# Kernel tuning notes

Measured on AMD Instinct MI355X. Metric: run time of the kernel, lower is better.

Reference implementation:

```python
import jax, jax.numpy as jnp
import numpy as np

B, S, HID = 1, 2048, 2048
H, KVH, HD = 16, 8, 128          # query heads, kv heads, head_dim = HID//H
N_REP = H // KVH                 # GQA expansion factor
EPS = 1e-6
THETA = 1e6
SCALING = HD ** (-0.5)           # note: original DIVIDES scores by this (bug kept)


def setup_inputs() -> dict:
    key = jax.random.key(0)
    ks = jax.random.split(key, 5)
    hidden_states = jax.random.normal(ks[0], (B, S, HID), jnp.float32)
    std = 0.02
    wq = jax.random.normal(ks[1], (HID, H * HD), jnp.float32) * std
    wk = jax.random.normal(ks[2], (HID, KVH * HD), jnp.float32) * std
    wv = jax.random.normal(ks[3], (HID, KVH * HD), jnp.float32) * std
    wo = jax.random.normal(ks[4], (H * HD, HID), jnp.float32) * std
    # RoPE tables as in Qwen3: inv_freq over even dims, emb = [freqs, freqs]
    pos = np.arange(S, dtype=np.float64)
    inv_freq = THETA ** (-np.arange(0, HD, 2, dtype=np.float64) / HD)
    freqs = pos[:, None] * inv_freq[None, :]            # [S, HD/2]
    emb = np.concatenate([freqs, freqs], axis=-1)       # [S, HD]
    cos = jnp.asarray(np.cos(emb)[None], jnp.float32)   # [1, S, HD]
    sin = jnp.asarray(np.sin(emb)[None], jnp.float32)
    return {"hidden_states": hidden_states, "cos": cos, "sin": sin,
            "wq": wq, "wk": wk, "wv": wv, "wo": wo}


def _rmsnorm(x):
    # weightless RMSNorm (the module's RMSNorm never applies .weight)
    return x * jax.lax.rsqrt(jnp.mean(x * x, axis=-1, keepdims=True) + EPS)


def _rotate_half(x):
    x1, x2 = jnp.split(x, 2, axis=-1)
    return jnp.concatenate([-x2, x1], axis=-1)


def reference(hidden_states, cos, sin, wq, wk, wv, wo):
    # projections + per-head QK RMSNorm, then [B,H,S,D] layout
    q = _rmsnorm((hidden_states @ wq).reshape(B, S, H, HD)).transpose(0, 2, 1, 3)
    k = _rmsnorm((hidden_states @ wk).reshape(B, S, KVH, HD)).transpose(0, 2, 1, 3)
    v = (hidden_states @ wv).reshape(B, S, KVH, HD).transpose(0, 2, 1, 3)
    # RoPE (cos/sin unsqueezed at head dim)
    c = cos[:, None, :, :]   # [B,1,S,HD]
    s = sin[:, None, :, :]
    q = q * c + _rotate_half(q) * s
    k = k * c + _rotate_half(k) * s
    # GQA repeat_kv: each kv head repeated N_REP consecutive times
    k = jnp.repeat(k, N_REP, axis=1)   # [B,H,S,HD]
    v = jnp.repeat(v, N_REP, axis=1)
    # faithful: scores DIVIDED by head_dim**-0.5 (i.e. * sqrt(HD)); no causal mask
    scores = jnp.einsum('bhqd,bhkd->bhqk', q, k) / SCALING
    probs = jax.nn.softmax(scores, axis=-1)
    attn = jnp.einsum('bhqk,bhkd->bhqd', probs, v)
    out = attn.transpose(0, 2, 1, 3).reshape(B, S, H * HD) @ wo
    return out
```

## Files before the change

kernel.cpp:

```cpp
#include <hip/hip_runtime.h>
#include <hip/hip_bf16.h>
#include <math.h>

#define S 2048
#define HID 2048
#define NH 16
#define KVH 8
#define HD 128
#define EPS 1e-6f
#define QK_SCALE 11.313708498984760390f

typedef __attribute__((ext_vector_type(8))) short s16x8;
typedef __attribute__((ext_vector_type(4))) float f32x4;

__device__ __forceinline__ unsigned short f2bf(float f) {
  __hip_bfloat16 h = __float2bfloat16(f);
  return *(unsigned short*)&h;
}
__device__ __forceinline__ float bf2f(unsigned short u) {
  unsigned int x = ((unsigned int)u) << 16;
  return __builtin_bit_cast(float, x);
}

__device__ __forceinline__ void gload16(const void* g, void* l) {
  __builtin_amdgcn_global_load_lds(
      (const __attribute__((address_space(1))) void*)g,
      (__attribute__((address_space(3))) void*)l, 16, 0, 0);
}

__global__ __launch_bounds__(256) void f32_to_bf16_split(const float* __restrict__ in,
                                                         unsigned short* __restrict__ hi,
                                                         unsigned short* __restrict__ lo,
                                                         int n4) {
  const int i = blockIdx.x * 256 + threadIdx.x;
  if (i < n4) {
    const float4 v = *(const float4*)(in + (size_t)i * 4);
    ushort4 h, l;
    h.x = f2bf(v.x); l.x = f2bf(v.x - bf2f(h.x));
    h.y = f2bf(v.y); l.y = f2bf(v.y - bf2f(h.y));
    h.z = f2bf(v.z); l.z = f2bf(v.z - bf2f(h.z));
    h.w = f2bf(v.w); l.w = f2bf(v.w - bf2f(h.w));
    *(ushort4*)(hi + (size_t)i * 4) = h;
    *(ushort4*)(lo + (size_t)i * 4) = l;
  }
}

__global__ __launch_bounds__(256) void transpose_to_bf16(const float* __restrict__ in,
                                                         unsigned short* __restrict__ out,
                                                         int K, int N) {
  __shared__ float t[64][65];
  const int n0 = blockIdx.x * 64;
  const int k0 = blockIdx.y * 64;
  const int tid = threadIdx.x;

  for (int idx = tid; idx < 64 * 16; idx += 256) {
    const int r = idx >> 4;
    const int c4 = (idx & 15) * 4;
    const float4 v = *(const float4*)(in + (size_t)(k0 + r) * N + n0 + c4);
    t[r][c4 + 0] = v.x; t[r][c4 + 1] = v.y; t[r][c4 + 2] = v.z; t[r][c4 + 3] = v.w;
  }
  __syncthreads();
  for (int idx = tid; idx < 64 * 16; idx += 256) {
    const int a = idx >> 4;
    const int b4 = (idx & 15) * 4;
    ushort4 u;
    u.x = f2bf(t[b4 + 0][a]); u.y = f2bf(t[b4 + 1][a]);
    u.z = f2bf(t[b4 + 2][a]); u.w = f2bf(t[b4 + 3][a]);
    *(ushort4*)(out + (size_t)(n0 + a) * K + k0 + b4) = u;
  }
}

__global__ __launch_bounds__(256) void transpose_to_bf16_split(const float* __restrict__ in,
                                                               unsigned short* __restrict__ ohi,
                                                               unsigned short* __restrict__ olo,
                                                               int K, int N) {
  __shared__ float t[64][65];
  const int n0 = blockIdx.x * 64;
  const int k0 = blockIdx.y * 64;
  const int tid = threadIdx.x;

  for (int idx = tid; idx < 64 * 16; idx += 256) {
    const int r = idx >> 4;
    const int c4 = (idx & 15) * 4;
    const float4 v = *(const float4*)(in + (size_t)(k0 + r) * N + n0 + c4);
    t[r][c4 + 0] = v.x; t[r][c4 + 1] = v.y; t[r][c4 + 2] = v.z; t[r][c4 + 3] = v.w;
  }
  __syncthreads();
  for (int idx = tid; idx < 64 * 16; idx += 256) {
    const int a = idx >> 4;
    const int b4 = (idx & 15) * 4;
    ushort4 h, l;
#pragma unroll
    for (int q = 0; q < 4; ++q) {
      const float v = t[b4 + q][a];
      const unsigned short hu = f2bf(v);
      const unsigned short lu = f2bf(v - bf2f(hu));
      ((unsigned short*)&h)[q] = hu;
      ((unsigned short*)&l)[q] = lu;
    }
    *(ushort4*)(ohi + (size_t)(n0 + a) * K + k0 + b4) = h;
    *(ushort4*)(olo + (size_t)(n0 + a) * K + k0 + b4) = l;
  }
}

#define BK 32

__global__ __launch_bounds__(256) void gemm_split_bt64(const unsigned short* __restrict__ Ahi,
                                                       const unsigned short* __restrict__ Alo,
                                                       const unsigned short* __restrict__ Bhi,
                                                       const unsigned short* __restrict__ Blo,
                                                       float* __restrict__ C,
                                                       int M, int N, int K, int ldc) {
  __shared__ unsigned short AsH[128 * BK];
  __shared__ unsigned short AsL[128 * BK];
  __shared__ unsigned short BsH[64 * BK];
  __shared__ unsigned short BsL[64 * BK];

  const int tid = threadIdx.x;
  const int lane = tid & 63;
  const int wave = tid >> 6;
  const int m0 = blockIdx.y * 128;
  const int n0 = blockIdx.x * 64;

  const int qm = (wave >> 1) * 64;
  const int qn = (wave & 1) * 32;
  const int l15 = lane & 15;
  const int quad = lane >> 4;

  const int st_row = lane >> 2;
  const int st_col = (lane & 3) * 8;

  f32x4 acc[4][2] = {};

  for (int k0 = 0; k0 < K; k0 += BK) {
#pragma unroll
    for (int p = 0; p < 2; ++p) {
      const int rb = p * 64 + wave * 16;
      const size_t aoff = (size_t)(m0 + rb + st_row) * K + k0 + st_col;
      gload16(Ahi + aoff, &AsH[rb * BK]);
      gload16(Alo + aoff, &AsL[rb * BK]);
    }
    {
      const int rb = wave * 16;
      const size_t boff = (size_t)(n0 + rb + st_row) * K + k0 + st_col;
      gload16(Bhi + boff, &BsH[rb * BK]);
      gload16(Blo + boff, &BsL[rb * BK]);
    }
    __syncthreads();

    s16x8 ah[4], al[4], bh[2], bl[2];
#pragma unroll
    for (int i = 0; i < 4; ++i) {
      const int ro = (qm + i * 16 + l15) * BK + quad * 8;
      ah[i] = *(const s16x8*)&AsH[ro];
      al[i] = *(const s16x8*)&AsL[ro];
    }
#pragma unroll
    for (int j = 0; j < 2; ++j) {
      const int ro = (qn + j * 16 + l15) * BK + quad * 8;
      bh[j] = *(const s16x8*)&BsH[ro];
      bl[j] = *(const s16x8*)&BsL[ro];
    }
#pragma unroll
    for (int i = 0; i < 4; ++i)
#pragma unroll
      for (int j = 0; j < 2; ++j) {
        acc[i][j] = __builtin_amdgcn_mfma_f32_16x16x32_bf16(ah[i], bh[j], acc[i][j], 0, 0, 0);
        acc[i][j] = __builtin_amdgcn_mfma_f32_16x16x32_bf16(ah[i], bl[j], acc[i][j], 0, 0, 0);
        acc[i][j] = __builtin_amdgcn_mfma_f32_16x16x32_bf16(al[i], bh[j], acc[i][j], 0, 0, 0);
      }
    __syncthreads();
  }

#pragma unroll
  for (int i = 0; i < 4; ++i) {
    const int row_base = m0 + qm + i * 16 + quad * 4;
#pragma unroll
    for (int j = 0; j < 2; ++j) {
      const int col = n0 + qn + j * 16 + l15;
#pragma unroll
      for (int r = 0; r < 4; ++r)
        C[(size_t)(row_base + r) * ldc + col] = acc[i][j][r];
    }
  }
}

template <int MODE, typename OT>
__global__ __launch_bounds__(256) void gemm_bf16_6464(const unsigned short* __restrict__ A,
                                                      const unsigned short* __restrict__ Bt,
                                                      OT* __restrict__ C,
                                                      int M, int N, int K, int ldc) {
  __shared__ unsigned short As[64 * BK];
  __shared__ unsigned short Bs[64 * BK];

  const int tid = threadIdx.x;
  const int lane = tid & 63;
  const int wave = tid >> 6;
  const int m0 = blockIdx.y * 64;
  const int n0 = blockIdx.x * 64;

  const int qm = (wave >> 1) * 32;
  const int qn = (wave & 1) * 32;
  const int l15 = lane & 15;
  const int quad = lane >> 4;

  const int st_row = lane >> 2;
  const int st_col = (lane & 3) * 8;

  f32x4 acc[2][2] = {};

  for (int k0 = 0; k0 < K; k0 += BK) {
    {
      const int rb = wave * 16;
      gload16(A + (size_t)(m0 + rb + st_row) * K + k0 + st_col, &As[rb * BK]);
      gload16(Bt + (size_t)(n0 + rb + st_row) * K + k0 + st_col, &Bs[rb * BK]);
    }
    __syncthreads();

    s16x8 a[2], b[2];
#pragma unroll
    for (int i = 0; i < 2; ++i)
      a[i] = *(const s16x8*)&As[(qm + i * 16 + l15) * BK + quad * 8];
#pragma unroll
    for (int j = 0; j < 2; ++j)
      b[j] = *(const s16x8*)&Bs[(qn + j * 16 + l15) * BK + quad * 8];
#pragma unroll
    for (int i = 0; i < 2; ++i)
#pragma unroll
      for (int j = 0; j < 2; ++j)
        acc[i][j] = __builtin_amdgcn_mfma_f32_16x16x32_bf16(a[i], b[j], acc[i][j], 0, 0, 0);
    __syncthreads();
  }

#pragma unroll
  for (int i = 0; i < 2; ++i) {
    const int row_base = m0 + qm + i * 16 + quad * 4;
#pragma unroll
    for (int j = 0; j < 2; ++j) {
      const int col = n0 + qn + j * 16 + l15;
      if constexpr (MODE == 0) {
#pragma unroll
        for (int r = 0; r < 4; ++r)
          C[(size_t)(row_base + r) * ldc + col] = acc[i][j][r];
      } else {
        ushort4 u;
        u.x = f2bf(acc[i][j][0]); u.y = f2bf(acc[i][j][1]);
        u.z = f2bf(acc[i][j][2]); u.w = f2bf(acc[i][j][3]);
        *(ushort4*)((unsigned short*)C + (size_t)col * ldc + row_base) = u;
      }
    }
  }
}

__global__ __launch_bounds__(256) void rmsnorm_rope_split(const float* __restrict__ qk,
                                                          const float* __restrict__ cosb,
                                                          const float* __restrict__ sinb,
                                                          unsigned short* __restrict__ qh,
                                                          unsigned short* __restrict__ ql,
                                                          unsigned short* __restrict__ kh,
                                                          unsigned short* __restrict__ kl) {
  const int s = blockIdx.x;
  const int wave = threadIdx.x >> 6;
  const int lane = threadIdx.x & 63;
  const int hh = blockIdx.y * 4 + wave;
  const bool is_q = (hh < 16);
  const int col = is_q ? hh * HD : 2048 + (hh - 16) * HD;

  const float* row = qk + (size_t)s * 3072 + col;
  const float x1 = row[lane];
  const float x2 = row[lane + 64];

  float ss = x1 * x1 + x2 * x2;
  ss += __shfl_xor(ss, 1);
  ss += __shfl_xor(ss, 2);
  ss += __shfl_xor(ss, 4);
  ss += __shfl_xor(ss, 8);
  ss += __shfl_xor(ss, 16);
  ss += __shfl_xor(ss, 32);
  const float r = rsqrtf(ss / 128.f + EPS);

  const float c = cosb[(size_t)s * HD + lane];
  const float sn = sinb[(size_t)s * HD + lane];
  float o1 = x1 * r * c - x2 * r * sn;
  float o2 = x2 * r * c + x1 * r * sn;
  if (is_q) { o1 *= QK_SCALE; o2 *= QK_SCALE; }

  const unsigned short h1 = f2bf(o1), l1 = f2bf(o1 - bf2f(h1));
  const unsigned short h2 = f2bf(o2), l2 = f2bf(o2 - bf2f(h2));
  if (is_q) {
    const size_t base = (size_t)s * 2048 + hh * HD + lane;
    qh[base] = h1; ql[base] = l1;
    qh[base + 64] = h2; ql[base + 64] = l2;
  } else {
    const size_t base = (size_t)s * 1024 + (hh - 16) * HD + lane;
    kh[base] = h1; kl[base] = l1;
    kh[base + 64] = h2; kl[base + 64] = l2;
  }
}

#define FA_N 64
#define FA_NT (S / FA_N)

__global__ __launch_bounds__(512, 4) void attn_flash_mfma(const unsigned short* __restrict__ qh,
                                                          const unsigned short* __restrict__ ql,
                                                          const unsigned short* __restrict__ kh,
                                                          const unsigned short* __restrict__ kl,
                                                          const unsigned short* __restrict__ vt,
                                                          unsigned short* __restrict__ out) {
  const int h = blockIdx.y;
  const int kvh = h >> 1;
  const int m0 = blockIdx.x * 64;
  const int tid = threadIdx.x;
  const int lane = tid & 63;
  const int wave = tid >> 6;
  const int rg = wave >> 1;
  const int kg = wave & 1;
  const int l15 = lane & 15;
  const int quad = lane >> 4;

  __shared__ char smem[59392];
  unsigned short* Kh = (unsigned short*)(smem);
  unsigned short* Kl = (unsigned short*)(smem + 16384);
  unsigned short* Vt = (unsigned short*)(smem + 32768);
  unsigned short* Pt = (unsigned short*)(smem + 49152) + wave * 640;

  auto STAGE = [&](int nt) {
#pragma unroll
    for (int p = 0; p < 2; ++p) {
      const int kr = wave * 8 + p * 4 + (lane >> 4);
      const size_t ksrc = (size_t)(nt + kr) * 1024 + kvh * HD + ((lane & 15) ^ (kr & 15)) * 8;
      gload16(kh + ksrc, Kh + (wave * 8 + p * 4) * 128);
      gload16(kl + ksrc, Kl + (wave * 8 + p * 4) * 128);
      const int d = wave * 16 + p * 8 + (lane >> 3);
      const size_t vsrc = (size_t)(kvh * HD + d) * 2048 + nt + ((lane & 7) ^ (d & 7)) * 8;
      gload16(vt + vsrc, Vt + (wave * 16 + p * 8) * 64);
    }
  };

  s16x8 qah[4], qal[4];
  {
    const int qrow = m0 + rg * 16 + l15;
#pragma unroll
    for (int ks = 0; ks < 4; ++ks) {
      const size_t off = (size_t)qrow * 2048 + h * HD + ks * 32 + quad * 8;
      qah[ks] = *(const s16x8*)(qh + off);
      qal[ks] = *(const s16x8*)(ql + off);
    }
  }

  f32x4 O[8] = {};
  float m_i[4], l_i[4];
#pragma unroll
  for (int r = 0; r < 4; ++r) { m_i[r] = -1e30f; l_i[r] = 0.f; }

  for (int t = 0; t < FA_NT; ++t) {
    __syncthreads();
    STAGE(t * FA_N);
    __syncthreads();

    f32x4 sacc[2] = {};
    __builtin_amdgcn_s_setprio(1);
#pragma unroll
    for (int ks = 0; ks < 4; ++ks) {
      s16x8 bh[2], bl[2];
#pragma unroll
      for (int j = 0; j < 2; ++j) {
        const int row = kg * 32 + j * 16 + l15;
        const int ro = row * 128 + (((ks * 4 + quad) ^ l15) * 8);
        bh[j] = *(const s16x8*)&Kh[ro];
        bl[j] = *(const s16x8*)&Kl[ro];
      }
#pragma unroll
      for (int j = 0; j < 2; ++j) {
        sacc[j] = __builtin_amdgcn_mfma_f32_16x16x32_bf16(qah[ks], bh[j], sacc[j], 0, 0, 0);
        sacc[j] = __builtin_amdgcn_mfma_f32_16x16x32_bf16(qah[ks], bl[j], sacc[j], 0, 0, 0);
        sacc[j] = __builtin_amdgcn_mfma_f32_16x16x32_bf16(qal[ks], bh[j], sacc[j], 0, 0, 0);
      }
    }
    __builtin_amdgcn_s_setprio(0);

    float mt[4];
    float dmax = -1e30f;
#pragma unroll
    for (int r = 0; r < 4; ++r) {
      float m = fmaxf(sacc[0][r], sacc[1][r]);
      m = fmaxf(m, __shfl_xor(m, 1));
      m = fmaxf(m, __shfl_xor(m, 2));
      m = fmaxf(m, __shfl_xor(m, 4));
      m = fmaxf(m, __shfl_xor(m, 8));
      mt[r] = m;
      dmax = fmaxf(dmax, m - m_i[r]);
    }
    if (__any(dmax > 8.f)) {
#pragma unroll
      for (int r = 0; r < 4; ++r) {
        const float mnew = fmaxf(m_i[r], mt[r]);
        const float alpha = __expf(m_i[r] - mnew);
        m_i[r] = mnew;
        l_i[r] *= alpha;
#pragma unroll
        for (int jd = 0; jd < 8; ++jd) O[jd][r] *= alpha;
      }
    }
#pragma unroll
    for (int r = 0; r < 4; ++r) {
      const float p0 = __expf(sacc[0][r] - m_i[r]);
      const float p1 = __expf(sacc[1][r] - m_i[r]);
      l_i[r] += p0 + p1;
      const int prow = quad * 4 + r;
      Pt[prow * 40 + l15] = f2bf(p0);
      Pt[prow * 40 + 16 + l15] = f2bf(p1);
    }

    const s16x8 pa = *(const s16x8*)&Pt[l15 * 40 + quad * 8];
    __builtin_amdgcn_s_setprio(1);
#pragma unroll
    for (int jd = 0; jd < 8; ++jd) {
      const int d = jd * 16 + l15;
      const int cp = ((kg * 4 + quad) ^ (d & 7)) * 8;
      const s16x8 vb = *(const s16x8*)&Vt[d * 64 + cp];
      O[jd] = __builtin_amdgcn_mfma_f32_16x16x32_bf16(pa, vb, O[jd], 0, 0, 0);
    }
    __builtin_amdgcn_s_setprio(0);
  }

#pragma unroll
  for (int r = 0; r < 4; ++r) {
    float ls = l_i[r];
    ls += __shfl_xor(ls, 1);
    ls += __shfl_xor(ls, 2);
    ls += __shfl_xor(ls, 4);
    ls += __shfl_xor(ls, 8);
    l_i[r] = ls;
  }

  __syncthreads();
  float* Om = (float*)smem;
  float* ms = (float*)(smem + 32768);
  float* ls2 = (float*)(smem + 33024);

  if (kg == 1) {
#pragma unroll
    for (int r = 0; r < 4; ++r) {
      const int row = rg * 16 + quad * 4 + r;
      if (l15 == 0) { ms[row] = m_i[r]; ls2[row] = l_i[r]; }
#pragma unroll
      for (int jd = 0; jd < 8; ++jd)
        Om[(size_t)row * 128 + jd * 16 + l15] = O[jd][r];
    }
  }
  __syncthreads();
  if (kg == 0) {
#pragma unroll
    for (int r = 0; r < 4; ++r) {
      const int row = rg * 16 + quad * 4 + r;
      const float mB = ms[row];
      const float lB = ls2[row];
      const float mS = fmaxf(m_i[r], mB);
      const float aA = __expf(m_i[r] - mS);
      const float aB = __expf(mB - mS);
      const float inv = 1.f / (aA * l_i[r] + aB * lB);
      const int grow = m0 + row;
#pragma unroll
      for (int jd = 0; jd < 8; ++jd) {
        const float oB = Om[(size_t)row * 128 + jd * 16 + l15];
        out[(size_t)grow * 2048 + h * HD + jd * 16 + l15] =
            f2bf((aA * O[jd][r] + aB * oB) * inv);
      }
    }
  }
}

extern "C" void kernel_launch(void* const* d_in, const int* in_sizes, int n_in,
                              void* d_out, int out_size, void* d_ws, size_t ws_size,
                              hipStream_t stream) {
  const float* hidden = (const float*)d_in[0];
  const float* cosb   = (const float*)d_in[1];
  const float* sinb   = (const float*)d_in[2];
  const float* wq     = (const float*)d_in[3];
  const float* wk     = (const float*)d_in[4];
  const float* wv     = (const float*)d_in[5];
  const float* wo     = (const float*)d_in[6];
  float* out = (float*)d_out;

  char* w = (char*)d_ws;
  float* qk_buf           = (float*)(w);
  unsigned short* wqkT_hi = (unsigned short*)(w + (24u << 20));
  unsigned short* wqkT_lo = (unsigned short*)(w + (36u << 20));
  unsigned short* hid_hi  = (unsigned short*)(w + (48u << 20));
  unsigned short* hid_lo  = (unsigned short*)(w + (56u << 20));
  unsigned short* vt_b    = (unsigned short*)(w + (64u << 20));
  unsigned short* wvT     = (unsigned short*)(w + (68u << 20));
  unsigned short* q_hi    = (unsigned short*)(w + (24u << 20));
  unsigned short* q_lo    = (unsigned short*)(w + (32u << 20));
  unsigned short* k_hi    = (unsigned short*)(w + (40u << 20));
  unsigned short* k_lo    = (unsigned short*)(w + (44u << 20));
  unsigned short* woT     = (unsigned short*)(w + (48u << 20));
  unsigned short* a_b     = (unsigned short*)(w + (56u << 20));

  dim3 blk(256);

  f32_to_bf16_split<<<dim3((S * HID / 4 + 255) / 256), blk, 0, stream>>>(hidden, hid_hi, hid_lo, S * HID / 4);
  transpose_to_bf16_split<<<dim3(32, 32), blk, 0, stream>>>(wq, wqkT_hi, wqkT_lo, HID, 2048);
  transpose_to_bf16_split<<<dim3(16, 32), blk, 0, stream>>>(wk, wqkT_hi + (size_t)2048 * 2048,
                                                            wqkT_lo + (size_t)2048 * 2048, HID, 1024);
  transpose_to_bf16<<<dim3(16, 32), blk, 0, stream>>>(wv, wvT, 2048, 1024);

  gemm_split_bt64<<<dim3(3072 / 64, S / 128), blk, 0, stream>>>(hid_hi, hid_lo, wqkT_hi, wqkT_lo,
                                                                qk_buf, S, 3072, HID, 3072);

  gemm_bf16_6464<1, unsigned short><<<dim3(1024 / 64, S / 64), blk, 0, stream>>>(
      hid_hi, wvT, vt_b, S, 1024, HID, 2048);

  transpose_to_bf16<<<dim3(32, 32), blk, 0, stream>>>(wo, woT, 2048, HID);

  rmsnorm_rope_split<<<dim3(S, 6), blk, 0, stream>>>(qk_buf, cosb, sinb, q_hi, q_lo, k_hi, k_lo);

  attn_flash_mfma<<<dim3(S / 64, NH), dim3(512), 0, stream>>>(q_hi, q_lo, k_hi, k_lo, vt_b, a_b);

  gemm_bf16_6464<0, float><<<dim3(HID / 64, S / 64), blk, 0, stream>>>(
      a_b, woT, out, S, HID, 2048, HID);
}
```

Before: 385.9 us.

## Fuse QK RMSNorm and RoPE into the split-bf16 QK projection GEMM epilogue

Retiles the Q/K projection GEMM so each block owns one full 128-wide head for 64 rows. The accumulator is staged through shared memory so the per-head RMSNorm, RoPE, scaling and hi/lo bf16 split run in the epilogue. This removes the fp32 intermediate buffer write/read and the separate normalization kernel launch. The trade-offs are a serial per-wave epilogue and a changed tile shape, which may affect GEMM efficiency.

```diff
diff --git a/kernel.cpp b/kernel.cpp
--- a/kernel.cpp
+++ b/kernel.cpp
@@ -105,66 +105,72 @@
 
 #define BK 32
 
-__global__ __launch_bounds__(256) void gemm_split_bt64(const unsigned short* __restrict__ Ahi,
-                                                       const unsigned short* __restrict__ Alo,
-                                                       const unsigned short* __restrict__ Bhi,
-                                                       const unsigned short* __restrict__ Blo,
-                                                       float* __restrict__ C,
-                                                       int M, int N, int K, int ldc) {
-  __shared__ unsigned short AsH[128 * BK];
-  __shared__ unsigned short AsL[128 * BK];
-  __shared__ unsigned short BsH[64 * BK];
-  __shared__ unsigned short BsL[64 * BK];
+__global__ __launch_bounds__(256) void gemm_qk_fused(const unsigned short* __restrict__ Ahi,
+                                                     const unsigned short* __restrict__ Alo,
+                                                     const unsigned short* __restrict__ Bhi,
+                                                     const unsigned short* __restrict__ Blo,
+                                                     const float* __restrict__ cosb,
+                                                     const float* __restrict__ sinb,
+                                                     unsigned short* __restrict__ qh,
+                                                     unsigned short* __restrict__ ql,
+                                                     unsigned short* __restrict__ kh,
+                                                     unsigned short* __restrict__ kl) {
+  __shared__ char smem[64 * 132 * 4];
+  unsigned short* AsH = (unsigned short*)smem;
+  unsigned short* AsL = (unsigned short*)(smem + 4096);
+  unsigned short* BsH = (unsigned short*)(smem + 8192);
+  unsigned short* BsL = (unsigned short*)(smem + 16384);
+  float* Sf = (float*)smem;
 
   const int tid = threadIdx.x;
   const int lane = tid & 63;
   const int wave = tid >> 6;
-  const int m0 = blockIdx.y * 128;
-  const int n0 = blockIdx.x * 64;
-
-  const int qm = (wave >> 1) * 64;
-  const int qn = (wave & 1) * 32;
+  const int hh = blockIdx.x;
+  const int m0 = blockIdx.y * 64;
+  const int n0 = hh * 128;
+
+  const int qm = (wave >> 1) * 32;
+  const int qn = (wave & 1) * 64;
   const int l15 = lane & 15;
   const int quad = lane >> 4;
-
   const int st_row = lane >> 2;
   const int st_col = (lane & 3) * 8;
 
-  f32x4 acc[4][2] = {};
-
-  for (int k0 = 0; k0 < K; k0 += BK) {
+  f32x4 acc[2][4] = {};
+
+  for (int k0 = 0; k0 < HID; k0 += BK) {
+    {
+      const int rb = wave * 16;
+      const size_t aoff = (size_t)(m0 + rb + st_row) * HID + k0 + st_col;
+      gload16(Ahi + aoff, &AsH[rb * BK]);
+      gload16(Alo + aoff, &AsL[rb * BK]);
+    }
 #pragma unroll
     for (int p = 0; p < 2; ++p) {
       const int rb = p * 64 + wave * 16;
-      const size_t aoff = (size_t)(m0 + rb + st_row) * K + k0 + st_col;
-      gload16(Ahi + aoff, &AsH[rb * BK]);
-      gload16(Alo + aoff, &AsL[rb * BK]);
-    }
-    {
-      const int rb = wave * 16;
-      const size_t boff = (size_t)(n0 + rb + st_row) * K + k0 + st_col;
+      const size_t boff = (size_t)(n0 + rb + st_row) * HID + k0 + st_col;
       gload16(Bhi + boff, &BsH[rb * BK]);
       gload16(Blo + boff, &BsL[rb * BK]);
     }
     __syncthreads();
 
-    s16x8 ah[4], al[4], bh[2], bl[2];
-#pragma unroll
-    for (int i = 0; i < 4; ++i) {
+    s16x8 ah[2], al[2], bh[4], bl[4];
+#pragma unroll
+    for (int i = 0; i < 2; ++i) {
       const int ro = (qm + i * 16 + l15) * BK + quad * 8;
       ah[i] = *(const s16x8*)&AsH[ro];
       al[i] = *(const s16x8*)&AsL[ro];
     }
 #pragma unroll
-    for (int j = 0; j < 2; ++j) {
+    for (int j = 0; j < 4; ++j) {
       const int ro = (qn + j * 16 + l15) * BK + quad * 8;
       bh[j] = *(const s16x8*)&BsH[ro];
       bl[j] = *(const s16x8*)&BsL[ro];
     }
 #pragma unroll
-    for (int i = 0; i < 4; ++i)
-#pragma unroll
-      for (int j = 0; j < 2; ++j) {
+    for (int i = 0; i < 2; ++i)
+#pragma unroll
+      for (int j = 0; j < 4; ++j) {
         acc[i][j] = __builtin_amdgcn_mfma_f32_16x16x32_bf16(ah[i], bh[j], acc[i][j], 0, 0, 0);
         acc[i][j] = __builtin_amdgcn_mfma_f32_16x16x32_bf16(ah[i], bl[j], acc[i][j], 0, 0, 0);
         acc[i][j] = __builtin_amdgcn_mfma_f32_16x16x32_bf16(al[i], bh[j], acc[i][j], 0, 0, 0);
@@ -173,14 +179,50 @@
   }
 
 #pragma unroll
-  for (int i = 0; i < 4; ++i) {
-    const int row_base = m0 + qm + i * 16 + quad * 4;
-#pragma unroll
-    for (int j = 0; j < 2; ++j) {
-      const int col = n0 + qn + j * 16 + l15;
+  for (int i = 0; i < 2; ++i) {
+    const int rbase = qm + i * 16 + quad * 4;
+#pragma unroll
+    for (int j = 0; j < 4; ++j) {
+      const int col = qn + j * 16 + l15;
 #pragma unroll
       for (int r = 0; r < 4; ++r)
-        C[(size_t)(row_base + r) * ldc + col] = acc[i][j][r];
+        Sf[(rbase + r) * 132 + col] = acc[i][j][r];
+    }
+  }
+  __syncthreads();
+
+  const bool is_q = (hh < 16);
+  for (int rr = 0; rr < 16; ++rr) {
+    const int row = wave * 16 + rr;
+    const int s = m0 + row;
+    const float x1 = Sf[row * 132 + lane];
+    const float x2 = Sf[row * 132 + 64 + lane];
+
+    float ss = x1 * x1 + x2 * x2;
+    ss += __shfl_xor(ss, 1);
+    ss += __shfl_xor(ss, 2);
+    ss += __shfl_xor(ss, 4);
+    ss += __shfl_xor(ss, 8);
+    ss += __shfl_xor(ss, 16);
+    ss += __shfl_xor(ss, 32);
+    const float rn = rsqrtf(ss / 128.f + EPS);
+
+    const float c = cosb[(size_t)s * HD + lane];
+    const float sn = sinb[(size_t)s * HD + lane];
+    float o1 = x1 * rn * c - x2 * rn * sn;
+    float o2 = x2 * rn * c + x1 * rn * sn;
+    if (is_q) { o1 *= QK_SCALE; o2 *= QK_SCALE; }
+
+    const unsigned short h1 = f2bf(o1), l1 = f2bf(o1 - bf2f(h1));
+    const unsigned short h2 = f2bf(o2), l2 = f2bf(o2 - bf2f(h2));
+    if (is_q) {
+      const size_t base = (size_t)s * 2048 + hh * HD + lane;
+      qh[base] = h1; ql[base] = l1;
+      qh[base + 64] = h2; ql[base + 64] = l2;
+    } else {
+      const size_t base = (size_t)s * 1024 + (hh - 16) * HD + lane;
+      kh[base] = h1; kl[base] = l1;
+      kh[base + 64] = h2; kl[base + 64] = l2;
     }
   }
 }
@@ -249,52 +291,6 @@
         *(ushort4*)((unsigned short*)C + (size_t)col * ldc + row_base) = u;
       }
     }
-  }
-}
-
-__global__ __launch_bounds__(256) void rmsnorm_rope_split(const float* __restrict__ qk,
-                                                          const float* __restrict__ cosb,
-                                                          const float* __restrict__ sinb,
-                                                          unsigned short* __restrict__ qh,
-                                                          unsigned short* __restrict__ ql,
-                                                          unsigned short* __restrict__ kh,
-                                                          unsigned short* __restrict__ kl) {
-  const int s = blockIdx.x;
-  const int wave = threadIdx.x >> 6;
-  const int lane = threadIdx.x & 63;
-  const int hh = blockIdx.y * 4 + wave;
-  const bool is_q = (hh < 16);
-  const int col = is_q ? hh * HD : 2048 + (hh - 16) * HD;
-
-  const float* row = qk + (size_t)s * 3072 + col;
-  const float x1 = row[lane];
-  const float x2 = row[lane + 64];
-
-  float ss = x1 * x1 + x2 * x2;
-  ss += __shfl_xor(ss, 1);
-  ss += __shfl_xor(ss, 2);
-  ss += __shfl_xor(ss, 4);
-  ss += __shfl_xor(ss, 8);
-  ss += __shfl_xor(ss, 16);
-  ss += __shfl_xor(ss, 32);
-  const float r = rsqrtf(ss / 128.f + EPS);
-
-  const float c = cosb[(size_t)s * HD + lane];
-  const float sn = sinb[(size_t)s * HD + lane];
-  float o1 = x1 * r * c - x2 * r * sn;
-  float o2 = x2 * r * c + x1 * r * sn;
-  if (is_q) { o1 *= QK_SCALE; o2 *= QK_SCALE; }
-
-  const unsigned short h1 = f2bf(o1), l1 = f2bf(o1 - bf2f(h1));
-  const unsigned short h2 = f2bf(o2), l2 = f2bf(o2 - bf2f(h2));
-  if (is_q) {
-    const size_t base = (size_t)s * 2048 + hh * HD + lane;
-    qh[base] = h1; ql[base] = l1;
-    qh[base + 64] = h2; ql[base + 64] = l2;
-  } else {
-    const size_t base = (size_t)s * 1024 + (hh - 16) * HD + lane;
-    kh[base] = h1; kl[base] = l1;
-    kh[base + 64] = h2; kl[base + 64] = l2;
   }
 }
 
@@ -484,17 +480,16 @@
   float* out = (float*)d_out;
 
   char* w = (char*)d_ws;
-  float* qk_buf           = (float*)(w);
+  unsigned short* q_hi    = (unsigned short*)(w);
+  unsigned short* q_lo    = (unsigned short*)(w + (8u << 20));
+  unsigned short* k_hi    = (unsigned short*)(w + (16u << 20));
+  unsigned short* k_lo    = (unsigned short*)(w + (20u << 20));
   unsigned short* wqkT_hi = (unsigned short*)(w + (24u << 20));
   unsigned short* wqkT_lo = (unsigned short*)(w + (36u << 20));
   unsigned short* hid_hi  = (unsigned short*)(w + (48u << 20));
   unsigned short* hid_lo  = (unsigned short*)(w + (56u << 20));
   unsigned short* vt_b    = (unsigned short*)(w + (64u << 20));
   unsigned short* wvT     = (unsigned short*)(w + (68u << 20));
-  unsigned short* q_hi    = (unsigned short*)(w + (24u << 20));
-  unsigned short* q_lo    = (unsigned short*)(w + (32u << 20));
-  unsigned short* k_hi    = (unsigned short*)(w + (40u << 20));
-  unsigned short* k_lo    = (unsigned short*)(w + (44u << 20));
   unsigned short* woT     = (unsigned short*)(w + (48u << 20));
   unsigned short* a_b     = (unsigned short*)(w + (56u << 20));
 
@@ -506,16 +501,14 @@
                                                             wqkT_lo + (size_t)2048 * 2048, HID, 1024);
   transpose_to_bf16<<<dim3(16, 32), blk, 0, stream>>>(wv, wvT, 2048, 1024);
 
-  gemm_split_bt64<<<dim3(3072 / 64, S / 128), blk, 0, stream>>>(hid_hi, hid_lo, wqkT_hi, wqkT_lo,
-                                                                qk_buf, S, 3072, HID, 3072);
+  gemm_qk_fused<<<dim3(24, 32), blk, 0, stream>>>(hid_hi, hid_lo, wqkT_hi, wqkT_lo,
+                                                  cosb, sinb, q_hi, q_lo, k_hi, k_lo);
 
   gemm_bf16_6464<1, unsigned short><<<dim3(1024 / 64, S / 64), blk, 0, stream>>>(
       hid_hi, wvT, vt_b, S, 1024, HID, 2048);
 
   transpose_to_bf16<<<dim3(32, 32), blk, 0, stream>>>(wo, woT, 2048, HID);
 
-  rmsnorm_rope_split<<<dim3(S, 6), blk, 0, stream>>>(qk_buf, cosb, sinb, q_hi, q_lo, k_hi, k_lo);
-
   attn_flash_mfma<<<dim3(S / 64, NH), dim3(512), 0, stream>>>(q_hi, q_lo, k_hi, k_lo, vt_b, a_b);
 
   gemm_bf16_6464<0, float><<<dim3(HID / 64, S / 64), blk, 0, stream>>>(
```

Measured after the change: 386.5 us. Within noise of the previous version (+0.2%).
